# Optimization experiments

Hardware: AMD Instinct MI355X
Metric: run time of the kernel (lower is better)

The kernel has to match this reference:

```python
import jax, jax.numpy as jnp
import numpy as np

B_, T_, M_, R_, S_ = 2, 2048, 768, 64, 16
LOG_EPS = float(np.log(1e-10))

def setup_inputs() -> dict:
    key = jax.random.key(0)
    ks = jax.random.split(key, 8)
    u = jax.random.normal(ks[0], (B_, T_, M_), jnp.float32)
    delta = jax.random.normal(ks[1], (B_, T_, R_), jnp.float32)
    # dt_proj weights kept small and bias strongly negative so softplus(dt) is
    # small -> cumulative log-decay over T=2048 stays in a numerically safe range
    dt_w = jax.random.normal(ks[2], (M_, R_), jnp.float32) * 1e-3
    dt_b = -8.0 + 0.1 * jax.random.normal(ks[3], (M_,), jnp.float32)
    # A_log ~ Uniform(-3, -1) as in nn.init.uniform_(self.A_log, -3.0, -1.0)
    A_log = jax.random.uniform(ks[4], (S_, M_), jnp.float32, minval=-3.0, maxval=-1.0)
    # xavier_uniform with gain=0.1 ~ small weights
    B_w = jax.random.normal(ks[5], (S_, M_), jnp.float32) * 0.005
    C_w = jax.random.normal(ks[6], (S_, M_), jnp.float32) * 0.005
    D = jnp.ones((M_,), jnp.float32)
    return dict(u=u, delta=delta, dt_w=dt_w, dt_b=dt_b, A_log=A_log, B_w=B_w, C_w=C_w, D=D)

def reference(u, delta, dt_w, dt_b, A_log, B_w, C_w, D):
    # delta = clamp(softplus(dt_proj(delta)))            [b,t,m]
    dt = jax.nn.softplus(jnp.einsum('btr,mr->btm', delta, dt_w) + dt_b)
    dt = jnp.clip(dt, 1e-6, 10.0)
    # A = clamp(-exp(A_log))                             [s,m]
    A = jnp.clip(-jnp.exp(A_log), -10.0, -1e-6)
    Bm = jnp.einsum('btm,sm->bts', u, B_w)               # B_proj(u)
    Cm = jnp.einsum('btm,sm->bts', u, C_w)               # C_proj(u)
    # discretization: deltaA = dt * A, deltaB_u = dt * B * u   [b,t,s,m]
    dA = dt[:, :, None, :] * A                           # log of exp(dt*A)
    dBu = dt[:, :, None, :] * Bm[..., None] * u[:, :, None, :]
    # associative scan via cumsum in log space (module's clamp(1e-10) -> floor log)
    cum_log_A = jnp.cumsum(jnp.maximum(dA, LOG_EPS), axis=1)   # [b,t,s,m]
    A_cum = jnp.exp(cum_log_A)
    # h_t = (prod_{k<=t} a_k) * sum_{k<=t} x_k / (prod_{j<=k} a_j)
    h = A_cum * jnp.cumsum(dBu * jnp.exp(-cum_log_A), axis=1)  # [b,t,s,m]
    y = jnp.einsum('btsm,bts->btm', h, Cm)
    out = jnp.clip(y + u * D, -1e4, 1e4)
    # module's NaN/Inf fallback to zeros, expressed jit-compatibly
    bad = jnp.any(~jnp.isfinite(out))
    return jnp.where(bad, jnp.zeros_like(out), out)
```

## Files before the change

kernel.cpp:

```cpp
#include <hip/hip_runtime.h>
#include <math.h>

#define B_ 2
#define T_ 2048
#define M_ 768
#define R_ 64
#define S_ 16
#define MS_ (M_ * S_)
#define NC 128
#define CL (T_ / NC)
#define LOG_EPS_F (-23.025850929940457f)

__global__ __launch_bounds__(256) void dt_kernel(
    const float* __restrict__ delta,
    const float* __restrict__ dt_w,
    const float* __restrict__ dt_b,
    float* __restrict__ dt_out)
{
  __shared__ float ds_d[R_][68];
  __shared__ float ds_w[R_][68];
  const int tid = threadIdx.x;
  const int m0  = blockIdx.x * 64;
  const int bt0 = blockIdx.y * 64;

  #pragma unroll
  for (int k = 0; k < 4; ++k) {
    int idx = tid + k * 256;
    int rq = idx & 15;
    int x  = idx >> 4;
    float4 dv = *reinterpret_cast<const float4*>(&delta[(size_t)(bt0 + x) * R_ + rq * 4]);
    ds_d[rq * 4 + 0][x] = dv.x; ds_d[rq * 4 + 1][x] = dv.y;
    ds_d[rq * 4 + 2][x] = dv.z; ds_d[rq * 4 + 3][x] = dv.w;
    float4 wv = *reinterpret_cast<const float4*>(&dt_w[(size_t)(m0 + x) * R_ + rq * 4]);
    ds_w[rq * 4 + 0][x] = wv.x; ds_w[rq * 4 + 1][x] = wv.y;
    ds_w[rq * 4 + 2][x] = wv.z; ds_w[rq * 4 + 3][x] = wv.w;
  }
  __syncthreads();

  const int mq = tid & 15, tq = tid >> 4;
  const int ml = mq * 4, tl = tq * 4;
  float acc[4][4] = {};
  #pragma unroll 4
  for (int r = 0; r < R_; ++r) {
    float4 dv = *reinterpret_cast<const float4*>(&ds_d[r][tl]);
    float4 wv = *reinterpret_cast<const float4*>(&ds_w[r][ml]);
    float d[4] = {dv.x, dv.y, dv.z, dv.w};
    float w[4] = {wv.x, wv.y, wv.z, wv.w};
    #pragma unroll
    for (int i = 0; i < 4; ++i)
      #pragma unroll
      for (int j = 0; j < 4; ++j)
        acc[i][j] = fmaf(d[i], w[j], acc[i][j]);
  }

  float4 bb = *reinterpret_cast<const float4*>(&dt_b[m0 + ml]);
  float bv[4] = {bb.x, bb.y, bb.z, bb.w};
  #pragma unroll
  for (int i = 0; i < 4; ++i) {
    float4 o;
    float* op = &o.x;
    #pragma unroll
    for (int j = 0; j < 4; ++j) {
      float x = acc[i][j] + bv[j];
      float sp = (x > 20.f) ? x : __logf(1.f + __expf(x));
      op[j] = fminf(fmaxf(sp, 1e-6f), 10.f);
    }
    *reinterpret_cast<float4*>(&dt_out[(size_t)(bt0 + tl + i) * M_ + m0 + ml]) = o;
  }
}

__global__ __launch_bounds__(512, 4) void bc_kernel(
    const float* __restrict__ u,
    const float* __restrict__ B_w,
    const float* __restrict__ C_w,
    float* __restrict__ Bm,
    float* __restrict__ Cm)
{
  const int wave = threadIdx.x >> 6, lane = threadIdx.x & 63;
  const int bt0 = blockIdx.x * 8;

  float4 w[4][3];
  #pragma unroll
  for (int s = 0; s < 4; ++s) {
    const int s_g = wave * 4 + s;
    const float* wr = (s_g < 16) ? &B_w[(size_t)s_g * M_] : &C_w[(size_t)(s_g - 16) * M_];
    const float4* w4 = reinterpret_cast<const float4*>(wr);
    w[s][0] = w4[lane]; w[s][1] = w4[64 + lane]; w[s][2] = w4[128 + lane];
  }

  float acc[32];
  #pragma unroll
  for (int r = 0; r < 8; ++r) {
    const float4* ur = reinterpret_cast<const float4*>(&u[(size_t)(bt0 + r) * M_]);
    const float4 a0 = ur[lane], a1 = ur[64 + lane], a2 = ur[128 + lane];
    #pragma unroll
    for (int s = 0; s < 4; ++s) {
      float t = 0.f;
      t = fmaf(a0.x, w[s][0].x, t); t = fmaf(a0.y, w[s][0].y, t);
      t = fmaf(a0.z, w[s][0].z, t); t = fmaf(a0.w, w[s][0].w, t);
      t = fmaf(a1.x, w[s][1].x, t); t = fmaf(a1.y, w[s][1].y, t);
      t = fmaf(a1.z, w[s][1].z, t); t = fmaf(a1.w, w[s][1].w, t);
      t = fmaf(a2.x, w[s][2].x, t); t = fmaf(a2.y, w[s][2].y, t);
      t = fmaf(a2.z, w[s][2].z, t); t = fmaf(a2.w, w[s][2].w, t);
      acc[r * 4 + s] = t;
    }
  }

  #pragma unroll
  for (int j = 0; j < 32; ++j) acc[j] += __shfl_xor(acc[j], 32);
  int cnt = 32;
  #pragma unroll
  for (int mask = 16; mask >= 1; mask >>= 1) {
    cnt >>= 1;
    const bool up = (lane & mask) != 0;
    #pragma unroll
    for (int j = 0; j < cnt; ++j) {
      float give = up ? acc[j] : acc[j + cnt];
      float keep = up ? acc[j + cnt] : acc[j];
      acc[j] = keep + __shfl_xor(give, mask);
    }
  }

  if (lane < 32) {
    const int r = lane >> 2, s_l = lane & 3;
    const int s_g = wave * 4 + s_l;
    const int bt = bt0 + r;
    if (s_g < 16) Bm[(size_t)bt * S_ + s_g] = acc[0];
    else          Cm[(size_t)bt * S_ + (s_g - 16)] = acc[0];
  }
}

template <int PHASE>
__global__ __launch_bounds__(128) void scan_kernel(
    const float* __restrict__ dt_ws,
    const float* __restrict__ u,
    const float* __restrict__ Bm,
    const float* __restrict__ Cm,
    const float* __restrict__ A_log,
    const float* __restrict__ D,
    float* __restrict__ Aprod,
    float* __restrict__ Hend,
    float* __restrict__ out)
{
  __shared__ float dt_lds[CL][64];
  __shared__ float u_lds[CL][64];
  __shared__ float lds_bm[CL * S_];
  __shared__ float lds_cm[CL * S_];

  const int tid = threadIdx.x;
  const int lane = tid & 63, wv = tid >> 6;
  const int m_l = wv * 32 + (lane & 31);
  const int sh = lane >> 5, s0 = sh * 8;
  const int m = blockIdx.x * 64 + m_l;
  const int c = blockIdx.y, b = blockIdx.z;
  const int t0 = c * CL;

  const size_t gbase = ((size_t)b * T_ + t0) * M_ + blockIdx.x * 64;
  #pragma unroll
  for (int p = 0; p < CL * 16 / 128; ++p) {
    const int i4 = tid + p * 128;
    const int t = i4 >> 4, m4 = (i4 & 15) * 4;
    *reinterpret_cast<float4*>(&dt_lds[t][m4]) =
        *reinterpret_cast<const float4*>(&dt_ws[gbase + (size_t)t * M_ + m4]);
    *reinterpret_cast<float4*>(&u_lds[t][m4]) =
        *reinterpret_cast<const float4*>(&u[gbase + (size_t)t * M_ + m4]);
  }
  {
    const size_t bcb = ((size_t)b * T_ + t0) * S_;
    #pragma unroll
    for (int p = 0; p < CL * S_ / 128; ++p) {
      const int idx = tid + p * 128;
      lds_bm[idx] = Bm[bcb + idx];
      if constexpr (PHASE == 3) lds_cm[idx] = Cm[bcb + idx];
    }
  }

  float Acol[8];
  #pragma unroll
  for (int s = 0; s < 8; ++s) {
    float a = -__expf(A_log[(size_t)(s0 + s) * M_ + m]);
    Acol[s] = fminf(fmaxf(a, -10.f), -1e-6f);
  }

  float h[8], P[8], Dm = 0.f;
  const size_t smb = (((size_t)b * NC + c) * S_ + s0) * M_ + m;
  if constexpr (PHASE == 1) {
    #pragma unroll
    for (int s = 0; s < 8; ++s) { h[s] = 0.f; P[s] = 1.f; }
  } else {
    #pragma unroll
    for (int s = 0; s < 8; ++s) h[s] = Aprod[smb + (size_t)s * M_];
    Dm = D[m];
  }

  __syncthreads();

  const size_t g0 = ((size_t)b * T_ + t0) * M_ + m;
  #pragma unroll 8
  for (int t = 0; t < CL; ++t) {
    const float dtv = dt_lds[t][m_l];
    const float uv  = u_lds[t][m_l];
    const float du  = dtv * uv;
    const float4 bv0 = *reinterpret_cast<const float4*>(&lds_bm[t * S_ + s0]);
    const float4 bv1 = *reinterpret_cast<const float4*>(&lds_bm[t * S_ + s0 + 4]);
    const float bmv[8] = {bv0.x, bv0.y, bv0.z, bv0.w, bv1.x, bv1.y, bv1.z, bv1.w};
    float cmv[8];
    if constexpr (PHASE == 3) {
      const float4 cv0 = *reinterpret_cast<const float4*>(&lds_cm[t * S_ + s0]);
      const float4 cv1 = *reinterpret_cast<const float4*>(&lds_cm[t * S_ + s0 + 4]);
      cmv[0] = cv0.x; cmv[1] = cv0.y; cmv[2] = cv0.z; cmv[3] = cv0.w;
      cmv[4] = cv1.x; cmv[5] = cv1.y; cmv[6] = cv1.z; cmv[7] = cv1.w;
    }
    float y = 0.f;
    #pragma unroll
    for (int s = 0; s < 8; ++s) {
      float la = fmaxf(dtv * Acol[s], LOG_EPS_F);
      float e = __expf(la);
      h[s] = fmaf(e, h[s], du * bmv[s]);
      if constexpr (PHASE == 1) P[s] *= e;
      else y = fmaf(h[s], cmv[s], y);
    }
    if constexpr (PHASE == 3) {
      y += __shfl_xor(y, 32);
      if (sh == 0) {
        float o = y + uv * Dm;
        out[g0 + (size_t)t * M_] = fminf(fmaxf(o, -1e4f), 1e4f);
      }
    }
  }

  if constexpr (PHASE == 1) {
    #pragma unroll
    for (int s = 0; s < 8; ++s) {
      Aprod[smb + (size_t)s * M_] = P[s];
      Hend[smb + (size_t)s * M_]  = h[s];
    }
  }
}

__global__ __launch_bounds__(256) void carry_kernel(
    float* __restrict__ Aprod, const float* __restrict__ Hend)
{
  const int idx = blockIdx.x * 256 + threadIdx.x;
  const int b = idx / MS_;
  const int sm = idx - b * MS_;
  float h = 0.f;
  #pragma unroll 16
  for (int c = 0; c < NC; ++c) {
    const size_t o = ((size_t)b * NC + c) * MS_ + sm;
    const float a  = Aprod[o];
    const float he = Hend[o];
    Aprod[o] = h;
    h = fmaf(a, h, he);
  }
}

extern "C" void kernel_launch(void* const* d_in, const int* in_sizes, int n_in,
                              void* d_out, int out_size, void* d_ws, size_t ws_size,
                              hipStream_t stream)
{
  const float* u     = (const float*)d_in[0];
  const float* delta = (const float*)d_in[1];
  const float* dt_w  = (const float*)d_in[2];
  const float* dt_b  = (const float*)d_in[3];
  const float* A_log = (const float*)d_in[4];
  const float* B_w   = (const float*)d_in[5];
  const float* C_w   = (const float*)d_in[6];
  const float* D     = (const float*)d_in[7];
  float* out = (float*)d_out;
  float* ws  = (float*)d_ws;

  const size_t fl_dt = (size_t)B_ * T_ * M_;
  const size_t fl_bc = (size_t)B_ * T_ * S_;
  const size_t fl_sm = (size_t)B_ * NC * MS_;

  float* dt_ws = ws;
  float* Bm    = dt_ws + fl_dt;
  float* Cm    = Bm + fl_bc;
  float* Aprod = Cm + fl_bc;
  float* Hend  = Aprod + fl_sm;

  dt_kernel<<<dim3(M_ / 64, (B_ * T_) / 64), 256, 0, stream>>>(delta, dt_w, dt_b, dt_ws);
  bc_kernel<<<dim3((B_ * T_) / 8), 512, 0, stream>>>(u, B_w, C_w, Bm, Cm);
  scan_kernel<1><<<dim3(M_ / 64, NC, B_), 128, 0, stream>>>(
      dt_ws, u, Bm, Cm, A_log, D, Aprod, Hend, nullptr);
  carry_kernel<<<dim3((B_ * MS_) / 256), 256, 0, stream>>>(Aprod, Hend);
  scan_kernel<3><<<dim3(M_ / 64, NC, B_), 128, 0, stream>>>(
      dt_ws, u, Bm, Cm, A_log, D, Aprod, Hend, out);
}
```

Before: 70.32 us.

## Fuse dt, B/C projection, chunked scan and carry into one cooperative kernel

```diff
diff --git a/kernel.cpp b/kernel.cpp
--- a/kernel.cpp
+++ b/kernel.cpp
@@ -1,5 +1,8 @@
 #include <hip/hip_runtime.h>
+#include <hip/hip_cooperative_groups.h>
 #include <math.h>
+
+namespace cg = cooperative_groups;
 
 #define B_ 2
 #define T_ 2048
@@ -7,22 +10,244 @@
 #define R_ 64
 #define S_ 16
 #define MS_ (M_ * S_)
-#define NC 128
-#define CL (T_ / NC)
 #define LOG_EPS_F (-23.025850929940457f)
 
+#define FNC 64
+#define FCL 32
+#define MT  128
+#define NMT 6
+#define FGRID (B_ * FNC * NMT)
+#define PITCH 132
+
+__global__ __launch_bounds__(256, 3) void fused_kernel(
+    const float* __restrict__ u, const float* __restrict__ delta,
+    const float* __restrict__ dt_w, const float* __restrict__ dt_b,
+    const float* __restrict__ A_log, const float* __restrict__ B_w,
+    const float* __restrict__ C_w, const float* __restrict__ D,
+    float* __restrict__ out,
+    float* __restrict__ part,
+    float* __restrict__ Bm_g,
+    float* __restrict__ Cm_g,
+    float* __restrict__ Aprod,
+    float* __restrict__ Hend)
+{
+  __shared__ float u_lds[FCL][PITCH];
+  __shared__ float dt_lds[FCL][PITCH];
+  __shared__ float scratch[4224];
+
+  cg::grid_group grid = cg::this_grid();
+
+  const int tid = threadIdx.x;
+  const int bid = blockIdx.x;
+  const int mt  = bid % NMT;
+  const int bc  = bid / NMT;
+  const int m0  = mt * MT;
+  const size_t row0 = (size_t)bc * FCL;
+
+  {
+    float (*delta_s)[68] = reinterpret_cast<float (*)[68]>(scratch);
+    #pragma unroll
+    for (int p = 0; p < 2; ++p) {
+      const int i4 = tid + p * 256;
+      const int t = i4 >> 4, c4 = (i4 & 15) * 4;
+      *reinterpret_cast<float4*>(&delta_s[t][c4]) =
+          *reinterpret_cast<const float4*>(&delta[(row0 + t) * R_ + c4]);
+    }
+    #pragma unroll
+    for (int p = 0; p < 4; ++p) {
+      const int i4 = tid + p * 256;
+      const int t = i4 >> 5, c4 = (i4 & 31) * 4;
+      *reinterpret_cast<float4*>(&u_lds[t][c4]) =
+          *reinterpret_cast<const float4*>(&u[(row0 + t) * M_ + m0 + c4]);
+    }
+  }
+  __syncthreads();
+
+  {
+    float (*delta_s)[68] = reinterpret_cast<float (*)[68]>(scratch);
+    const int ml = tid & 127, th = tid >> 7;
+    float acc[16] = {};
+    const float* wrow = &dt_w[(size_t)(m0 + ml) * R_];
+    #pragma unroll
+    for (int r4 = 0; r4 < R_; r4 += 4) {
+      const float4 w4 = *reinterpret_cast<const float4*>(&wrow[r4]);
+      #pragma unroll
+      for (int i = 0; i < 16; ++i) {
+        const float4 d4 = *reinterpret_cast<const float4*>(&delta_s[th * 16 + i][r4]);
+        acc[i] = fmaf(d4.x, w4.x, acc[i]);
+        acc[i] = fmaf(d4.y, w4.y, acc[i]);
+        acc[i] = fmaf(d4.z, w4.z, acc[i]);
+        acc[i] = fmaf(d4.w, w4.w, acc[i]);
+      }
+    }
+    const float bias = dt_b[m0 + ml];
+    #pragma unroll
+    for (int i = 0; i < 16; ++i) {
+      const float x = acc[i] + bias;
+      const float sp = (x > 20.f) ? x : __logf(1.f + __expf(x));
+      dt_lds[th * 16 + i][ml] = fminf(fmaxf(sp, 1e-6f), 10.f);
+    }
+  }
+  __syncthreads();
+
+  {
+    float (*W_lds)[PITCH] = reinterpret_cast<float (*)[PITCH]>(scratch);
+    #pragma unroll
+    for (int p = 0; p < 4; ++p) {
+      const int i4 = tid + p * 256;
+      const int s2 = i4 >> 5, c4 = (i4 & 31) * 4;
+      const float* src = (s2 < 16) ? &B_w[(size_t)s2 * M_] : &C_w[(size_t)(s2 - 16) * M_];
+      *reinterpret_cast<float4*>(&W_lds[s2][c4]) =
+          *reinterpret_cast<const float4*>(&src[m0 + c4]);
+    }
+  }
+  __syncthreads();
+
+  {
+    float (*W_lds)[PITCH] = reinterpret_cast<float (*)[PITCH]>(scratch);
+    const int t = tid >> 3, sq = tid & 7;
+    float acc[4] = {};
+    #pragma unroll
+    for (int k4 = 0; k4 < MT; k4 += 4) {
+      const float4 uv = *reinterpret_cast<const float4*>(&u_lds[t][k4]);
+      #pragma unroll
+      for (int j = 0; j < 4; ++j) {
+        const float4 wv = *reinterpret_cast<const float4*>(&W_lds[sq + 8 * j][k4]);
+        acc[j] = fmaf(uv.x, wv.x, acc[j]);
+        acc[j] = fmaf(uv.y, wv.y, acc[j]);
+        acc[j] = fmaf(uv.z, wv.z, acc[j]);
+        acc[j] = fmaf(uv.w, wv.w, acc[j]);
+      }
+    }
+    #pragma unroll
+    for (int j = 0; j < 4; ++j) {
+      const int s2 = sq + 8 * j;
+      part[(((size_t)bc * FCL + t) * 32 + s2) * 8 + mt] = acc[j];
+    }
+  }
+  grid.sync();
+
+  if (mt == 0) {
+    for (int o = tid; o < FCL * 32; o += 256) {
+      const int t = o >> 5, s2 = o & 31;
+      const float* p = &part[(((size_t)bc * FCL + t) * 32 + s2) * 8];
+      const float v = ((p[0] + p[1]) + (p[2] + p[3])) + (p[4] + p[5]);
+      const size_t bt = row0 + t;
+      if (s2 < 16) Bm_g[bt * S_ + s2] = v;
+      else         Cm_g[bt * S_ + (s2 - 16)] = v;
+    }
+  }
+  grid.sync();
+
+  float* bm_lds = scratch;
+  float* cm_lds = scratch + 512;
+  for (int idx = tid; idx < FCL * S_; idx += 256) {
+    bm_lds[idx] = Bm_g[row0 * S_ + idx];
+    cm_lds[idx] = Cm_g[row0 * S_ + idx];
+  }
+
+  const int ml = (tid >> 6) * 32 + (tid & 31);
+  const int sh = (tid >> 5) & 1, s0 = sh * 8;
+  const int m = m0 + ml;
+
+  float Acol[8];
+  #pragma unroll
+  for (int s = 0; s < 8; ++s) {
+    const float a = -__expf(A_log[(size_t)(s0 + s) * M_ + m]);
+    Acol[s] = fminf(fmaxf(a, -10.f), -1e-6f);
+  }
+  __syncthreads();
+
+  const size_t smb = ((size_t)bc * S_ + s0) * M_ + m;
+  {
+    float h[8], P[8];
+    #pragma unroll
+    for (int s = 0; s < 8; ++s) { h[s] = 0.f; P[s] = 1.f; }
+    #pragma unroll 8
+    for (int t = 0; t < FCL; ++t) {
+      const float dtv = dt_lds[t][ml];
+      const float uv  = u_lds[t][ml];
+      const float du  = dtv * uv;
+      const float4 bv0 = *reinterpret_cast<const float4*>(&bm_lds[t * S_ + s0]);
+      const float4 bv1 = *reinterpret_cast<const float4*>(&bm_lds[t * S_ + s0 + 4]);
+      const float bmv[8] = {bv0.x, bv0.y, bv0.z, bv0.w, bv1.x, bv1.y, bv1.z, bv1.w};
+      #pragma unroll
+      for (int s = 0; s < 8; ++s) {
+        const float la = fmaxf(dtv * Acol[s], LOG_EPS_F);
+        const float e = __expf(la);
+        h[s] = fmaf(e, h[s], du * bmv[s]);
+        P[s] *= e;
+      }
+    }
+    #pragma unroll
+    for (int s = 0; s < 8; ++s) {
+      Aprod[smb + (size_t)s * M_] = P[s];
+      Hend[smb + (size_t)s * M_]  = h[s];
+    }
+  }
+  grid.sync();
+
+  if (bid < (B_ * MS_) / 256) {
+    const int idx = bid * 256 + tid;
+    const int b2 = idx / MS_;
+    const int sm = idx - b2 * MS_;
+    float h = 0.f;
+    #pragma unroll 8
+    for (int cc = 0; cc < FNC; ++cc) {
+      const size_t o = ((size_t)b2 * FNC + cc) * MS_ + sm;
+      const float a  = Aprod[o];
+      const float he = Hend[o];
+      Aprod[o] = h;
+      h = fmaf(a, h, he);
+    }
+  }
+  grid.sync();
+
+  {
+    float h[8];
+    #pragma unroll
+    for (int s = 0; s < 8; ++s) h[s] = Aprod[smb + (size_t)s * M_];
+    const float Dm = D[m];
+    #pragma unroll 8
+    for (int t = 0; t < FCL; ++t) {
+      const float dtv = dt_lds[t][ml];
+      const float uv  = u_lds[t][ml];
+      const float du  = dtv * uv;
+      const float4 bv0 = *reinterpret_cast<const float4*>(&bm_lds[t * S_ + s0]);
+      const float4 bv1 = *reinterpret_cast<const float4*>(&bm_lds[t * S_ + s0 + 4]);
+      const float bmv[8] = {bv0.x, bv0.y, bv0.z, bv0.w, bv1.x, bv1.y, bv1.z, bv1.w};
+      const float4 cv0 = *reinterpret_cast<const float4*>(&cm_lds[t * S_ + s0]);
+      const float4 cv1 = *reinterpret_cast<const float4*>(&cm_lds[t * S_ + s0 + 4]);
+      const float cmv[8] = {cv0.x, cv0.y, cv0.z, cv0.w, cv1.x, cv1.y, cv1.z, cv1.w};
+      float y = 0.f;
+      #pragma unroll
+      for (int s = 0; s < 8; ++s) {
+        const float la = fmaxf(dtv * Acol[s], LOG_EPS_F);
+        const float e = __expf(la);
+        h[s] = fmaf(e, h[s], du * bmv[s]);
+        y = fmaf(h[s], cmv[s], y);
+      }
+      y += __shfl_xor(y, 32);
+      if (sh == 0) {
+        const float o = y + uv * Dm;
+        out[(row0 + t) * M_ + m] = fminf(fmaxf(o, -1e4f), 1e4f);
+      }
+    }
+  }
+}
+
+#define NCF 128
+#define CLF (T_ / NCF)
+
 __global__ __launch_bounds__(256) void dt_kernel(
-    const float* __restrict__ delta,
-    const float* __restrict__ dt_w,
-    const float* __restrict__ dt_b,
-    float* __restrict__ dt_out)
+    const float* __restrict__ delta, const float* __restrict__ dt_w,
+    const float* __restrict__ dt_b, float* __restrict__ dt_out)
 {
   __shared__ float ds_d[R_][68];
   __shared__ float ds_w[R_][68];
   const int tid = threadIdx.x;
   const int m0  = blockIdx.x * 64;
   const int bt0 = blockIdx.y * 64;
-
   #pragma unroll
   for (int k = 0; k < 4; ++k) {
     int idx = tid + k * 256;
@@ -36,14 +261,13 @@
     ds_w[rq * 4 + 2][x] = wv.z; ds_w[rq * 4 + 3][x] = wv.w;
   }
   __syncthreads();
-
   const int mq = tid & 15, tq = tid >> 4;
-  const int ml = mq * 4, tl = tq * 4;
+  const int mlq = mq * 4, tl = tq * 4;
   float acc[4][4] = {};
   #pragma unroll 4
   for (int r = 0; r < R_; ++r) {
     float4 dv = *reinterpret_cast<const float4*>(&ds_d[r][tl]);
-    float4 wv = *reinterpret_cast<const float4*>(&ds_w[r][ml]);
+    float4 wv = *reinterpret_cast<const float4*>(&ds_w[r][mlq]);
     float d[4] = {dv.x, dv.y, dv.z, dv.w};
     float w[4] = {wv.x, wv.y, wv.z, wv.w};
     #pragma unroll
@@ -52,8 +276,7 @@
       for (int j = 0; j < 4; ++j)
         acc[i][j] = fmaf(d[i], w[j], acc[i][j]);
   }
-
-  float4 bb = *reinterpret_cast<const float4*>(&dt_b[m0 + ml]);
+  float4 bb = *reinterpret_cast<const float4*>(&dt_b[m0 + mlq]);
   float bv[4] = {bb.x, bb.y, bb.z, bb.w};
   #pragma unroll
   for (int i = 0; i < 4; ++i) {
@@ -65,20 +288,16 @@
       float sp = (x > 20.f) ? x : __logf(1.f + __expf(x));
       op[j] = fminf(fmaxf(sp, 1e-6f), 10.f);
     }
-    *reinterpret_cast<float4*>(&dt_out[(size_t)(bt0 + tl + i) * M_ + m0 + ml]) = o;
+    *reinterpret_cast<float4*>(&dt_out[(size_t)(bt0 + tl + i) * M_ + m0 + mlq]) = o;
   }
 }
 
 __global__ __launch_bounds__(512, 4) void bc_kernel(
-    const float* __restrict__ u,
-    const float* __restrict__ B_w,
-    const float* __restrict__ C_w,
-    float* __restrict__ Bm,
-    float* __restrict__ Cm)
+    const float* __restrict__ u, const float* __restrict__ B_w,
+    const float* __restrict__ C_w, float* __restrict__ Bm, float* __restrict__ Cm)
 {
   const int wave = threadIdx.x >> 6, lane = threadIdx.x & 63;
   const int bt0 = blockIdx.x * 8;
-
   float4 w[4][3];
   #pragma unroll
   for (int s = 0; s < 4; ++s) {
@@ -87,7 +306,6 @@
     const float4* w4 = reinterpret_cast<const float4*>(wr);
     w[s][0] = w4[lane]; w[s][1] = w4[64 + lane]; w[s][2] = w4[128 + lane];
   }
-
   float acc[32];
   #pragma unroll
   for (int r = 0; r < 8; ++r) {
@@ -105,7 +323,6 @@
       acc[r * 4 + s] = t;
     }
   }
-
   #pragma unroll
   for (int j = 0; j < 32; ++j) acc[j] += __shfl_xor(acc[j], 32);
   int cnt = 32;
@@ -120,7 +337,6 @@
       acc[j] = keep + __shfl_xor(give, mask);
     }
   }
-
   if (lane < 32) {
     const int r = lane >> 2, s_l = lane & 3;
     const int s_g = wave * 4 + s_l;
@@ -132,32 +348,25 @@
 
 template <int PHASE>
 __global__ __launch_bounds__(128) void scan_kernel(
-    const float* __restrict__ dt_ws,
-    const float* __restrict__ u,
-    const float* __restrict__ Bm,
-    const float* __restrict__ Cm,
-    const float* __restrict__ A_log,
-    const float* __restrict__ D,
-    float* __restrict__ Aprod,
-    float* __restrict__ Hend,
-    float* __restrict__ out)
+    const float* __restrict__ dt_ws, const float* __restrict__ u,
+    const float* __restrict__ Bm, const float* __restrict__ Cm,
+    const float* __restrict__ A_log, const float* __restrict__ D,
+    float* __restrict__ Aprod, float* __restrict__ Hend, float* __restrict__ out)
 {
-  __shared__ float dt_lds[CL][64];
-  __shared__ float u_lds[CL][64];
-  __shared__ float lds_bm[CL * S_];
-  __shared__ float lds_cm[CL * S_];
-
+  __shared__ float dt_lds[CLF][64];
+  __shared__ float u_lds[CLF][64];
+  __shared__ float lds_bm[CLF * S_];
+  __shared__ float lds_cm[CLF * S_];
   const int tid = threadIdx.x;
   const int lane = tid & 63, wv = tid >> 6;
   const int m_l = wv * 32 + (lane & 31);
   const int sh = lane >> 5, s0 = sh * 8;
   const int m = blockIdx.x * 64 + m_l;
   const int c = blockIdx.y, b = blockIdx.z;
-  const int t0 = c * CL;
-
+  const int t0 = c * CLF;
   const size_t gbase = ((size_t)b * T_ + t0) * M_ + blockIdx.x * 64;
   #pragma unroll
-  for (int p = 0; p < CL * 16 / 128; ++p) {
+  for (int p = 0; p < CLF * 16 / 128; ++p) {
     const int i4 = tid + p * 128;
     const int t = i4 >> 4, m4 = (i4 & 15) * 4;
     *reinterpret_cast<float4*>(&dt_lds[t][m4]) =
@@ -168,22 +377,20 @@
   {
     const size_t bcb = ((size_t)b * T_ + t0) * S_;
     #pragma unroll
-    for (int p = 0; p < CL * S_ / 128; ++p) {
+    for (int p = 0; p < CLF * S_ / 128; ++p) {
       const int idx = tid + p * 128;
       lds_bm[idx] = Bm[bcb + idx];
       if constexpr (PHASE == 3) lds_cm[idx] = Cm[bcb + idx];
     }
   }
-
   float Acol[8];
   #pragma unroll
   for (int s = 0; s < 8; ++s) {
     float a = -__expf(A_log[(size_t)(s0 + s) * M_ + m]);
     Acol[s] = fminf(fmaxf(a, -10.f), -1e-6f);
   }
-
   float h[8], P[8], Dm = 0.f;
-  const size_t smb = (((size_t)b * NC + c) * S_ + s0) * M_ + m;
+  const size_t smb = (((size_t)b * NCF + c) * S_ + s0) * M_ + m;
   if constexpr (PHASE == 1) {
     #pragma unroll
     for (int s = 0; s < 8; ++s) { h[s] = 0.f; P[s] = 1.f; }
@@ -192,12 +399,10 @@
     for (int s = 0; s < 8; ++s) h[s] = Aprod[smb + (size_t)s * M_];
     Dm = D[m];
   }
-
   __syncthreads();
-
   const size_t g0 = ((size_t)b * T_ + t0) * M_ + m;
   #pragma unroll 8
-  for (int t = 0; t < CL; ++t) {
+  for (int t = 0; t < CLF; ++t) {
     const float dtv = dt_lds[t][m_l];
     const float uv  = u_lds[t][m_l];
     const float du  = dtv * uv;
@@ -228,7 +433,6 @@
       }
     }
   }
-
   if constexpr (PHASE == 1) {
     #pragma unroll
     for (int s = 0; s < 8; ++s) {
@@ -246,8 +450,8 @@
   const int sm = idx - b * MS_;
   float h = 0.f;
   #pragma unroll 16
-  for (int c = 0; c < NC; ++c) {
-    const size_t o = ((size_t)b * NC + c) * MS_ + sm;
+  for (int c = 0; c < NCF; ++c) {
+    const size_t o = ((size_t)b * NCF + c) * MS_ + sm;
     const float a  = Aprod[o];
     const float he = Hend[o];
     Aprod[o] = h;
@@ -270,21 +474,38 @@
   float* out = (float*)d_out;
   float* ws  = (float*)d_ws;
 
-  const size_t fl_dt = (size_t)B_ * T_ * M_;
-  const size_t fl_bc = (size_t)B_ * T_ * S_;
-  const size_t fl_sm = (size_t)B_ * NC * MS_;
-
-  float* dt_ws = ws;
-  float* Bm    = dt_ws + fl_dt;
-  float* Cm    = Bm + fl_bc;
-  float* Aprod = Cm + fl_bc;
-  float* Hend  = Aprod + fl_sm;
-
-  dt_kernel<<<dim3(M_ / 64, (B_ * T_) / 64), 256, 0, stream>>>(delta, dt_w, dt_b, dt_ws);
-  bc_kernel<<<dim3((B_ * T_) / 8), 512, 0, stream>>>(u, B_w, C_w, Bm, Cm);
-  scan_kernel<1><<<dim3(M_ / 64, NC, B_), 128, 0, stream>>>(
-      dt_ws, u, Bm, Cm, A_log, D, Aprod, Hend, nullptr);
-  carry_kernel<<<dim3((B_ * MS_) / 256), 256, 0, stream>>>(Aprod, Hend);
-  scan_kernel<3><<<dim3(M_ / 64, NC, B_), 128, 0, stream>>>(
-      dt_ws, u, Bm, Cm, A_log, D, Aprod, Hend, out);
+  int maxB = 0;
+  hipOccupancyMaxActiveBlocksPerMultiprocessor(&maxB, fused_kernel, 256, 0);
+  hipDeviceProp_t* unused = nullptr; (void)unused;
+  const bool coop_ok = (maxB * 256 >= FGRID);
+
+  if (coop_ok) {
+    float* part  = ws;
+    float* Bm_g  = part + (size_t)128 * FCL * 32 * 8;
+    float* Cm_g  = Bm_g + (size_t)B_ * T_ * S_;
+    float* Aprod = Cm_g + (size_t)B_ * T_ * S_;
+    float* Hend  = Aprod + (size_t)B_ * FNC * MS_;
+    void* args[] = {(void*)&u, (void*)&delta, (void*)&dt_w, (void*)&dt_b,
+                    (void*)&A_log, (void*)&B_w, (void*)&C_w, (void*)&D,
+                    (void*)&out, (void*)&part, (void*)&Bm_g, (void*)&Cm_g,
+                    (void*)&Aprod, (void*)&Hend};
+    hipLaunchCooperativeKernel((const void*)fused_kernel, dim3(FGRID), dim3(256),
+                               args, 0, stream);
+  } else {
+    const size_t fl_dt = (size_t)B_ * T_ * M_;
+    const size_t fl_bc = (size_t)B_ * T_ * S_;
+    const size_t fl_sm = (size_t)B_ * NCF * MS_;
+    float* dt_ws = ws;
+    float* Bm    = dt_ws + fl_dt;
+    float* Cm    = Bm + fl_bc;
+    float* Aprod = Cm + fl_bc;
+    float* Hend  = Aprod + fl_sm;
+    dt_kernel<<<dim3(M_ / 64, (B_ * T_) / 64), 256, 0, stream>>>(delta, dt_w, dt_b, dt_ws);
+    bc_kernel<<<dim3((B_ * T_) / 8), 512, 0, stream>>>(u, B_w, C_w, Bm, Cm);
+    scan_kernel<1><<<dim3(M_ / 64, NCF, B_), 128, 0, stream>>>(
+        dt_ws, u, Bm, Cm, A_log, D, Aprod, Hend, nullptr);
+    carry_kernel<<<dim3((B_ * MS_) / 256), 256, 0, stream>>>(Aprod, Hend);
+    scan_kernel<3><<<dim3(M_ / 64, NCF, B_), 128, 0, stream>>>(
+        dt_ws, u, Bm, Cm, A_log, D, Aprod, Hend, out);
+  }
 }
```

Measured after the change: 70.32 us. About the same (+0.0%).

## Fuse dt projection into scan kernels and halve chunk length

Applied to the files above, without the earlier changes.

```diff
diff --git a/kernel.cpp b/kernel.cpp
--- a/kernel.cpp
+++ b/kernel.cpp
@@ -7,67 +7,9 @@
 #define R_ 64
 #define S_ 16
 #define MS_ (M_ * S_)
-#define NC 128
-#define CL (T_ / NC)
+#define NC 64
+#define CL 32
 #define LOG_EPS_F (-23.025850929940457f)
-
-__global__ __launch_bounds__(256) void dt_kernel(
-    const float* __restrict__ delta,
-    const float* __restrict__ dt_w,
-    const float* __restrict__ dt_b,
-    float* __restrict__ dt_out)
-{
-  __shared__ float ds_d[R_][68];
-  __shared__ float ds_w[R_][68];
-  const int tid = threadIdx.x;
-  const int m0  = blockIdx.x * 64;
-  const int bt0 = blockIdx.y * 64;
-
-  #pragma unroll
-  for (int k = 0; k < 4; ++k) {
-    int idx = tid + k * 256;
-    int rq = idx & 15;
-    int x  = idx >> 4;
-    float4 dv = *reinterpret_cast<const float4*>(&delta[(size_t)(bt0 + x) * R_ + rq * 4]);
-    ds_d[rq * 4 + 0][x] = dv.x; ds_d[rq * 4 + 1][x] = dv.y;
-    ds_d[rq * 4 + 2][x] = dv.z; ds_d[rq * 4 + 3][x] = dv.w;
-    float4 wv = *reinterpret_cast<const float4*>(&dt_w[(size_t)(m0 + x) * R_ + rq * 4]);
-    ds_w[rq * 4 + 0][x] = wv.x; ds_w[rq * 4 + 1][x] = wv.y;
-    ds_w[rq * 4 + 2][x] = wv.z; ds_w[rq * 4 + 3][x] = wv.w;
-  }
-  __syncthreads();
-
-  const int mq = tid & 15, tq = tid >> 4;
-  const int ml = mq * 4, tl = tq * 4;
-  float acc[4][4] = {};
-  #pragma unroll 4
-  for (int r = 0; r < R_; ++r) {
-    float4 dv = *reinterpret_cast<const float4*>(&ds_d[r][tl]);
-    float4 wv = *reinterpret_cast<const float4*>(&ds_w[r][ml]);
-    float d[4] = {dv.x, dv.y, dv.z, dv.w};
-    float w[4] = {wv.x, wv.y, wv.z, wv.w};
-    #pragma unroll
-    for (int i = 0; i < 4; ++i)
-      #pragma unroll
-      for (int j = 0; j < 4; ++j)
-        acc[i][j] = fmaf(d[i], w[j], acc[i][j]);
-  }
-
-  float4 bb = *reinterpret_cast<const float4*>(&dt_b[m0 + ml]);
-  float bv[4] = {bb.x, bb.y, bb.z, bb.w};
-  #pragma unroll
-  for (int i = 0; i < 4; ++i) {
-    float4 o;
-    float* op = &o.x;
-    #pragma unroll
-    for (int j = 0; j < 4; ++j) {
-      float x = acc[i][j] + bv[j];
-      float sp = (x > 20.f) ? x : __logf(1.f + __expf(x));
-      op[j] = fminf(fmaxf(sp, 1e-6f), 10.f);
-    }
-    *reinterpret_cast<float4*>(&dt_out[(size_t)(bt0 + tl + i) * M_ + m0 + ml]) = o;
-  }
-}
 
 __global__ __launch_bounds__(512, 4) void bc_kernel(
     const float* __restrict__ u,
@@ -130,10 +72,14 @@
   }
 }
 
+#define DPITCH 72
+
 template <int PHASE>
-__global__ __launch_bounds__(128) void scan_kernel(
-    const float* __restrict__ dt_ws,
+__global__ __launch_bounds__(128) void scan_fused(
     const float* __restrict__ u,
+    const float* __restrict__ delta,
+    const float* __restrict__ dt_w,
+    const float* __restrict__ dt_b,
     const float* __restrict__ Bm,
     const float* __restrict__ Cm,
     const float* __restrict__ A_log,
@@ -142,43 +88,80 @@
     float* __restrict__ Hend,
     float* __restrict__ out)
 {
+  __shared__ float u_lds[CL][64];
   __shared__ float dt_lds[CL][64];
-  __shared__ float u_lds[CL][64];
-  __shared__ float lds_bm[CL * S_];
-  __shared__ float lds_cm[CL * S_];
+  __shared__ float scratch[CL * DPITCH];
 
   const int tid = threadIdx.x;
+  const int mt = blockIdx.x;
+  const int c  = blockIdx.y;
+  const int b  = blockIdx.z;
+  const int m0 = mt * 64;
+  const int t0 = c * CL;
+  const size_t row0 = (size_t)b * T_ + t0;
+
+  {
+    float (*delta_s)[DPITCH] = reinterpret_cast<float (*)[DPITCH]>(scratch);
+    #pragma unroll
+    for (int p = 0; p < 4; ++p) {
+      const int i4 = tid + p * 128;
+      const int t = i4 >> 4, c4 = (i4 & 15) * 4;
+      *reinterpret_cast<float4*>(&delta_s[t][c4]) =
+          *reinterpret_cast<const float4*>(&delta[(row0 + t) * R_ + c4]);
+      *reinterpret_cast<float4*>(&u_lds[t][c4]) =
+          *reinterpret_cast<const float4*>(&u[(row0 + t) * M_ + m0 + c4]);
+    }
+  }
+  __syncthreads();
+
+  {
+    float (*delta_s)[DPITCH] = reinterpret_cast<float (*)[DPITCH]>(scratch);
+    const int ml2 = tid & 63, th = tid >> 6;
+    float acc[16] = {};
+    const float* wrow = &dt_w[(size_t)(m0 + ml2) * R_];
+    #pragma unroll
+    for (int r4 = 0; r4 < R_; r4 += 4) {
+      const float4 w4 = *reinterpret_cast<const float4*>(&wrow[r4]);
+      #pragma unroll
+      for (int i = 0; i < 16; ++i) {
+        const float4 d4 = *reinterpret_cast<const float4*>(&delta_s[th * 16 + i][r4]);
+        acc[i] = fmaf(d4.x, w4.x, acc[i]);
+        acc[i] = fmaf(d4.y, w4.y, acc[i]);
+        acc[i] = fmaf(d4.z, w4.z, acc[i]);
+        acc[i] = fmaf(d4.w, w4.w, acc[i]);
+      }
+    }
+    const float bias = dt_b[m0 + ml2];
+    #pragma unroll
+    for (int i = 0; i < 16; ++i) {
+      const float x = acc[i] + bias;
+      const float sp = (x > 20.f) ? x : __logf(1.f + __expf(x));
+      dt_lds[th * 16 + i][ml2] = fminf(fmaxf(sp, 1e-6f), 10.f);
+    }
+  }
+  __syncthreads();
+
+  float* bm_lds = scratch;
+  float* cm_lds = scratch + CL * S_;
+  {
+    const size_t bcb = row0 * S_;
+    #pragma unroll
+    for (int p = 0; p < CL * S_ / 128; ++p) {
+      const int idx = tid + p * 128;
+      bm_lds[idx] = Bm[bcb + idx];
+      if constexpr (PHASE == 3) cm_lds[idx] = Cm[bcb + idx];
+    }
+  }
+
   const int lane = tid & 63, wv = tid >> 6;
   const int m_l = wv * 32 + (lane & 31);
   const int sh = lane >> 5, s0 = sh * 8;
-  const int m = blockIdx.x * 64 + m_l;
-  const int c = blockIdx.y, b = blockIdx.z;
-  const int t0 = c * CL;
-
-  const size_t gbase = ((size_t)b * T_ + t0) * M_ + blockIdx.x * 64;
-  #pragma unroll
-  for (int p = 0; p < CL * 16 / 128; ++p) {
-    const int i4 = tid + p * 128;
-    const int t = i4 >> 4, m4 = (i4 & 15) * 4;
-    *reinterpret_cast<float4*>(&dt_lds[t][m4]) =
-        *reinterpret_cast<const float4*>(&dt_ws[gbase + (size_t)t * M_ + m4]);
-    *reinterpret_cast<float4*>(&u_lds[t][m4]) =
-        *reinterpret_cast<const float4*>(&u[gbase + (size_t)t * M_ + m4]);
-  }
-  {
-    const size_t bcb = ((size_t)b * T_ + t0) * S_;
-    #pragma unroll
-    for (int p = 0; p < CL * S_ / 128; ++p) {
-      const int idx = tid + p * 128;
-      lds_bm[idx] = Bm[bcb + idx];
-      if constexpr (PHASE == 3) lds_cm[idx] = Cm[bcb + idx];
-    }
-  }
+  const int m = m0 + m_l;
 
   float Acol[8];
   #pragma unroll
   for (int s = 0; s < 8; ++s) {
-    float a = -__expf(A_log[(size_t)(s0 + s) * M_ + m]);
+    const float a = -__expf(A_log[(size_t)(s0 + s) * M_ + m]);
     Acol[s] = fminf(fmaxf(a, -10.f), -1e-6f);
   }
 
@@ -192,30 +175,28 @@
     for (int s = 0; s < 8; ++s) h[s] = Aprod[smb + (size_t)s * M_];
     Dm = D[m];
   }
-
   __syncthreads();
 
-  const size_t g0 = ((size_t)b * T_ + t0) * M_ + m;
   #pragma unroll 8
   for (int t = 0; t < CL; ++t) {
     const float dtv = dt_lds[t][m_l];
     const float uv  = u_lds[t][m_l];
     const float du  = dtv * uv;
-    const float4 bv0 = *reinterpret_cast<const float4*>(&lds_bm[t * S_ + s0]);
-    const float4 bv1 = *reinterpret_cast<const float4*>(&lds_bm[t * S_ + s0 + 4]);
+    const float4 bv0 = *reinterpret_cast<const float4*>(&bm_lds[t * S_ + s0]);
+    const float4 bv1 = *reinterpret_cast<const float4*>(&bm_lds[t * S_ + s0 + 4]);
     const float bmv[8] = {bv0.x, bv0.y, bv0.z, bv0.w, bv1.x, bv1.y, bv1.z, bv1.w};
     float cmv[8];
     if constexpr (PHASE == 3) {
-      const float4 cv0 = *reinterpret_cast<const float4*>(&lds_cm[t * S_ + s0]);
-      const float4 cv1 = *reinterpret_cast<const float4*>(&lds_cm[t * S_ + s0 + 4]);
+      const float4 cv0 = *reinterpret_cast<const float4*>(&cm_lds[t * S_ + s0]);
+      const float4 cv1 = *reinterpret_cast<const float4*>(&cm_lds[t * S_ + s0 + 4]);
       cmv[0] = cv0.x; cmv[1] = cv0.y; cmv[2] = cv0.z; cmv[3] = cv0.w;
       cmv[4] = cv1.x; cmv[5] = cv1.y; cmv[6] = cv1.z; cmv[7] = cv1.w;
     }
     float y = 0.f;
     #pragma unroll
     for (int s = 0; s < 8; ++s) {
-      float la = fmaxf(dtv * Acol[s], LOG_EPS_F);
-      float e = __expf(la);
+      const float la = fmaxf(dtv * Acol[s], LOG_EPS_F);
+      const float e = __expf(la);
       h[s] = fmaf(e, h[s], du * bmv[s]);
       if constexpr (PHASE == 1) P[s] *= e;
       else y = fmaf(h[s], cmv[s], y);
@@ -223,8 +204,8 @@
     if constexpr (PHASE == 3) {
       y += __shfl_xor(y, 32);
       if (sh == 0) {
-        float o = y + uv * Dm;
-        out[g0 + (size_t)t * M_] = fminf(fmaxf(o, -1e4f), 1e4f);
+        const float o = y + uv * Dm;
+        out[(row0 + t) * M_ + m] = fminf(fmaxf(o, -1e4f), 1e4f);
       }
     }
   }
@@ -270,21 +251,18 @@
   float* out = (float*)d_out;
   float* ws  = (float*)d_ws;
 
-  const size_t fl_dt = (size_t)B_ * T_ * M_;
   const size_t fl_bc = (size_t)B_ * T_ * S_;
   const size_t fl_sm = (size_t)B_ * NC * MS_;
 
-  float* dt_ws = ws;
-  float* Bm    = dt_ws + fl_dt;
+  float* Bm    = ws;
   float* Cm    = Bm + fl_bc;
   float* Aprod = Cm + fl_bc;
   float* Hend  = Aprod + fl_sm;
 
-  dt_kernel<<<dim3(M_ / 64, (B_ * T_) / 64), 256, 0, stream>>>(delta, dt_w, dt_b, dt_ws);
   bc_kernel<<<dim3((B_ * T_) / 8), 512, 0, stream>>>(u, B_w, C_w, Bm, Cm);
-  scan_kernel<1><<<dim3(M_ / 64, NC, B_), 128, 0, stream>>>(
-      dt_ws, u, Bm, Cm, A_log, D, Aprod, Hend, nullptr);
+  scan_fused<1><<<dim3(M_ / 64, NC, B_), 128, 0, stream>>>(
+      u, delta, dt_w, dt_b, Bm, Cm, A_log, D, Aprod, Hend, nullptr);
   carry_kernel<<<dim3((B_ * MS_) / 256), 256, 0, stream>>>(Aprod, Hend);
-  scan_kernel<3><<<dim3(M_ / 64, NC, B_), 128, 0, stream>>>(
-      dt_ws, u, Bm, Cm, A_log, D, Aprod, Hend, out);
-}
+  scan_fused<3><<<dim3(M_ / 64, NC, B_), 128, 0, stream>>>(
+      u, delta, dt_w, dt_b, Bm, Cm, A_log, D, Aprod, Hend, out);
+}
```

Result: slower. 89.84 us (+27.8%).

## Double scan chunk length with register-prefetched second half and exp2 decay

Applied to the files above, without the earlier changes.

```diff
diff --git a/kernel.cpp b/kernel.cpp
--- a/kernel.cpp
+++ b/kernel.cpp
@@ -7,9 +7,10 @@
 #define R_ 64
 #define S_ 16
 #define MS_ (M_ * S_)
-#define NC 128
-#define CL (T_ / NC)
-#define LOG_EPS_F (-23.025850929940457f)
+#define NC 64
+#define HL 16
+#define LOG2E 1.4426950408889634f
+#define LOG2_EPS (-33.219280948873623f)
 
 __global__ __launch_bounds__(256) void dt_kernel(
     const float* __restrict__ delta,
@@ -131,7 +132,7 @@
 }
 
 template <int PHASE>
-__global__ __launch_bounds__(128) void scan_kernel(
+__global__ __launch_bounds__(128) void scan_v6(
     const float* __restrict__ dt_ws,
     const float* __restrict__ u,
     const float* __restrict__ Bm,
@@ -142,97 +143,155 @@
     float* __restrict__ Hend,
     float* __restrict__ out)
 {
-  __shared__ float dt_lds[CL][64];
-  __shared__ float u_lds[CL][64];
-  __shared__ float lds_bm[CL * S_];
-  __shared__ float lds_cm[CL * S_];
+  __shared__ float u0_lds[HL][64], u1_lds[HL][64];
+  __shared__ float d0_lds[HL][64], d1_lds[HL][64];
+  __shared__ float bm0[HL * S_], bm1[HL * S_];
+  __shared__ float cm0[HL * S_], cm1[HL * S_];
 
   const int tid = threadIdx.x;
+  const int mt = blockIdx.x;
+  const int c  = blockIdx.y;
+  const int b  = blockIdx.z;
+  const int m0 = mt * 64;
+  const int t0 = c * 32;
+  const size_t row0 = (size_t)b * T_ + t0;
+
   const int lane = tid & 63, wv = tid >> 6;
   const int m_l = wv * 32 + (lane & 31);
   const int sh = lane >> 5, s0 = sh * 8;
-  const int m = blockIdx.x * 64 + m_l;
-  const int c = blockIdx.y, b = blockIdx.z;
-  const int t0 = c * CL;
-
-  const size_t gbase = ((size_t)b * T_ + t0) * M_ + blockIdx.x * 64;
-  #pragma unroll
-  for (int p = 0; p < CL * 16 / 128; ++p) {
-    const int i4 = tid + p * 128;
-    const int t = i4 >> 4, m4 = (i4 & 15) * 4;
-    *reinterpret_cast<float4*>(&dt_lds[t][m4]) =
-        *reinterpret_cast<const float4*>(&dt_ws[gbase + (size_t)t * M_ + m4]);
-    *reinterpret_cast<float4*>(&u_lds[t][m4]) =
-        *reinterpret_cast<const float4*>(&u[gbase + (size_t)t * M_ + m4]);
-  }
+  const int m = m0 + m_l;
+
+  const int st0 = tid >> 4, sm4 = (tid & 15) * 4;
+  const int st1 = (tid + 128) >> 4, sm41 = ((tid + 128) & 15) * 4;
+
+  *reinterpret_cast<float4*>(&u0_lds[st0][sm4]) =
+      *reinterpret_cast<const float4*>(&u[(row0 + st0) * M_ + m0 + sm4]);
+  *reinterpret_cast<float4*>(&u0_lds[st1][sm41]) =
+      *reinterpret_cast<const float4*>(&u[(row0 + st1) * M_ + m0 + sm41]);
+  *reinterpret_cast<float4*>(&d0_lds[st0][sm4]) =
+      *reinterpret_cast<const float4*>(&dt_ws[(row0 + st0) * M_ + m0 + sm4]);
+  *reinterpret_cast<float4*>(&d0_lds[st1][sm41]) =
+      *reinterpret_cast<const float4*>(&dt_ws[(row0 + st1) * M_ + m0 + sm41]);
   {
-    const size_t bcb = ((size_t)b * T_ + t0) * S_;
-    #pragma unroll
-    for (int p = 0; p < CL * S_ / 128; ++p) {
-      const int idx = tid + p * 128;
-      lds_bm[idx] = Bm[bcb + idx];
-      if constexpr (PHASE == 3) lds_cm[idx] = Cm[bcb + idx];
-    }
-  }
-
-  float Acol[8];
+    const size_t bcb = row0 * S_;
+    bm0[tid]       = Bm[bcb + tid];
+    bm0[tid + 128] = Bm[bcb + tid + 128];
+    if constexpr (PHASE == 3) {
+      cm0[tid]       = Cm[bcb + tid];
+      cm0[tid + 128] = Cm[bcb + tid + 128];
+    }
+  }
+
+  float A2[8];
   #pragma unroll
   for (int s = 0; s < 8; ++s) {
-    float a = -__expf(A_log[(size_t)(s0 + s) * M_ + m]);
-    Acol[s] = fminf(fmaxf(a, -10.f), -1e-6f);
-  }
-
-  float h[8], P[8], Dm = 0.f;
+    const float a = -__expf(A_log[(size_t)(s0 + s) * M_ + m]);
+    A2[s] = fminf(fmaxf(a, -10.f), -1e-6f) * LOG2E;
+  }
+  float h[8], Sla[8], Dm = 0.f;
   const size_t smb = (((size_t)b * NC + c) * S_ + s0) * M_ + m;
   if constexpr (PHASE == 1) {
     #pragma unroll
-    for (int s = 0; s < 8; ++s) { h[s] = 0.f; P[s] = 1.f; }
+    for (int s = 0; s < 8; ++s) { h[s] = 0.f; Sla[s] = 0.f; }
   } else {
     #pragma unroll
     for (int s = 0; s < 8; ++s) h[s] = Aprod[smb + (size_t)s * M_];
     Dm = D[m];
   }
-
   __syncthreads();
 
-  const size_t g0 = ((size_t)b * T_ + t0) * M_ + m;
-  #pragma unroll 8
-  for (int t = 0; t < CL; ++t) {
-    const float dtv = dt_lds[t][m_l];
-    const float uv  = u_lds[t][m_l];
+  const size_t row1 = row0 + HL;
+  const float4 pu0 = *reinterpret_cast<const float4*>(&u[(row1 + st0) * M_ + m0 + sm4]);
+  const float4 pu1 = *reinterpret_cast<const float4*>(&u[(row1 + st1) * M_ + m0 + sm41]);
+  const float4 pd0 = *reinterpret_cast<const float4*>(&dt_ws[(row1 + st0) * M_ + m0 + sm4]);
+  const float4 pd1 = *reinterpret_cast<const float4*>(&dt_ws[(row1 + st1) * M_ + m0 + sm41]);
+  const size_t bcb1 = row1 * S_;
+  const float pb0 = Bm[bcb1 + tid];
+  const float pb1 = Bm[bcb1 + tid + 128];
+  float pc0 = 0.f, pc1 = 0.f;
+  if constexpr (PHASE == 3) {
+    pc0 = Cm[bcb1 + tid];
+    pc1 = Cm[bcb1 + tid + 128];
+  }
+
+  #pragma unroll
+  for (int t = 0; t < HL; ++t) {
+    const float dtv = d0_lds[t][m_l];
+    const float uv  = u0_lds[t][m_l];
     const float du  = dtv * uv;
-    const float4 bv0 = *reinterpret_cast<const float4*>(&lds_bm[t * S_ + s0]);
-    const float4 bv1 = *reinterpret_cast<const float4*>(&lds_bm[t * S_ + s0 + 4]);
+    const float4 bv0 = *reinterpret_cast<const float4*>(&bm0[t * S_ + s0]);
+    const float4 bv1 = *reinterpret_cast<const float4*>(&bm0[t * S_ + s0 + 4]);
     const float bmv[8] = {bv0.x, bv0.y, bv0.z, bv0.w, bv1.x, bv1.y, bv1.z, bv1.w};
     float cmv[8];
     if constexpr (PHASE == 3) {
-      const float4 cv0 = *reinterpret_cast<const float4*>(&lds_cm[t * S_ + s0]);
-      const float4 cv1 = *reinterpret_cast<const float4*>(&lds_cm[t * S_ + s0 + 4]);
+      const float4 cv0 = *reinterpret_cast<const float4*>(&cm0[t * S_ + s0]);
+      const float4 cv1 = *reinterpret_cast<const float4*>(&cm0[t * S_ + s0 + 4]);
       cmv[0] = cv0.x; cmv[1] = cv0.y; cmv[2] = cv0.z; cmv[3] = cv0.w;
       cmv[4] = cv1.x; cmv[5] = cv1.y; cmv[6] = cv1.z; cmv[7] = cv1.w;
     }
     float y = 0.f;
     #pragma unroll
     for (int s = 0; s < 8; ++s) {
-      float la = fmaxf(dtv * Acol[s], LOG_EPS_F);
-      float e = __expf(la);
+      const float la = fmaxf(dtv * A2[s], LOG2_EPS);
+      const float e  = exp2f(la);
       h[s] = fmaf(e, h[s], du * bmv[s]);
-      if constexpr (PHASE == 1) P[s] *= e;
+      if constexpr (PHASE == 1) Sla[s] += la;
       else y = fmaf(h[s], cmv[s], y);
     }
     if constexpr (PHASE == 3) {
       y += __shfl_xor(y, 32);
       if (sh == 0) {
-        float o = y + uv * Dm;
-        out[g0 + (size_t)t * M_] = fminf(fmaxf(o, -1e4f), 1e4f);
+        const float o = y + uv * Dm;
+        out[(row0 + t) * M_ + m] = fminf(fmaxf(o, -1e4f), 1e4f);
       }
     }
   }
 
+  *reinterpret_cast<float4*>(&u1_lds[st0][sm4])  = pu0;
+  *reinterpret_cast<float4*>(&u1_lds[st1][sm41]) = pu1;
+  *reinterpret_cast<float4*>(&d1_lds[st0][sm4])  = pd0;
+  *reinterpret_cast<float4*>(&d1_lds[st1][sm41]) = pd1;
+  bm1[tid] = pb0; bm1[tid + 128] = pb1;
+  if constexpr (PHASE == 3) { cm1[tid] = pc0; cm1[tid + 128] = pc1; }
+  __syncthreads();
+
+  #pragma unroll
+  for (int t = 0; t < HL; ++t) {
+    const float dtv = d1_lds[t][m_l];
+    const float uv  = u1_lds[t][m_l];
+    const float du  = dtv * uv;
+    const float4 bv0 = *reinterpret_cast<const float4*>(&bm1[t * S_ + s0]);
+    const float4 bv1 = *reinterpret_cast<const float4*>(&bm1[t * S_ + s0 + 4]);
+    const float bmv[8] = {bv0.x, bv0.y, bv0.z, bv0.w, bv1.x, bv1.y, bv1.z, bv1.w};
+    float cmv[8];
+    if constexpr (PHASE == 3) {
+      const float4 cv0 = *reinterpret_cast<const float4*>(&cm1[t * S_ + s0]);
+      const float4 cv1 = *reinterpret_cast<const float4*>(&cm1[t * S_ + s0 + 4]);
+      cmv[0] = cv0.x; cmv[1] = cv0.y; cmv[2] = cv0.z; cmv[3] = cv0.w;
+      cmv[4] = cv1.x; cmv[5] = cv1.y; cmv[6] = cv1.z; cmv[7] = cv1.w;
+    }
+    float y = 0.f;
+    #pragma unroll
+    for (int s = 0; s < 8; ++s) {
+      const float la = fmaxf(dtv * A2[s], LOG2_EPS);
+      const float e  = exp2f(la);
+      h[s] = fmaf(e, h[s], du * bmv[s]);
+      if constexpr (PHASE == 1) Sla[s] += la;
+      else y = fmaf(h[s], cmv[s], y);
+    }
+    if constexpr (PHASE == 3) {
+      y += __shfl_xor(y, 32);
+      if (sh == 0) {
+        const float o = y + uv * Dm;
+        out[(row1 + t) * M_ + m] = fminf(fmaxf(o, -1e4f), 1e4f);
+      }
+    }
+  }
+
   if constexpr (PHASE == 1) {
     #pragma unroll
     for (int s = 0; s < 8; ++s) {
-      Aprod[smb + (size_t)s * M_] = P[s];
+      Aprod[smb + (size_t)s * M_] = exp2f(Sla[s]);
       Hend[smb + (size_t)s * M_]  = h[s];
     }
   }
@@ -282,9 +341,9 @@
 
   dt_kernel<<<dim3(M_ / 64, (B_ * T_) / 64), 256, 0, stream>>>(delta, dt_w, dt_b, dt_ws);
   bc_kernel<<<dim3((B_ * T_) / 8), 512, 0, stream>>>(u, B_w, C_w, Bm, Cm);
-  scan_kernel<1><<<dim3(M_ / 64, NC, B_), 128, 0, stream>>>(
+  scan_v6<1><<<dim3(M_ / 64, NC, B_), 128, 0, stream>>>(
       dt_ws, u, Bm, Cm, A_log, D, Aprod, Hend, nullptr);
   carry_kernel<<<dim3((B_ * MS_) / 256), 256, 0, stream>>>(Aprod, Hend);
-  scan_kernel<3><<<dim3(M_ / 64, NC, B_), 128, 0, stream>>>(
+  scan_v6<3><<<dim3(M_ / 64, NC, B_), 128, 0, stream>>>(
       dt_ws, u, Bm, Cm, A_log, D, Aprod, Hend, out);
 }
```

After: 85.31 us. 1.21x slower.
